# Kernel optimization log

Measured on AMD Instinct MI355X. Metric: run time of the kernel, lower is better.

## Reference

```python
import jax, jax.numpy as jnp
import numpy as np

DIM = 384
PATCH = [(4, 4), (8, 8), (16, 16)]  # (width, height) per channel chunk
B, H, W = 4, 192, 192


def setup_inputs() -> dict:
    key = jax.random.key(0)
    ks = jax.random.split(key, 6)
    c = DIM
    return {
        "rgb": jax.random.normal(ks[0], (B, c, H, W), jnp.float32),
        "fre": jax.random.normal(ks[1], (B, c, H, W), jnp.float32),
        # shared BatchNorm2d (eval-mode affine) applied to both rgb and fre
        "norm_gamma": jnp.ones((c,), jnp.float32),
        "norm_beta": jnp.zeros((c,), jnp.float32),
        "norm_mean": jnp.zeros((c,), jnp.float32),
        "norm_var": jnp.ones((c,), jnp.float32),
        # qv: Conv2d(c, 2c, 1); k: Conv2d(c, c, 1)
        "qv_w": jax.random.normal(ks[2], (2 * c, c), jnp.float32) * 0.02,
        "qv_b": jnp.zeros((2 * c,), jnp.float32),
        "k_w": jax.random.normal(ks[3], (c, c), jnp.float32) * 0.02,
        "k_b": jnp.zeros((c,), jnp.float32),
        # out_conv: Conv2d(c, c, 3, padding=1, bias=False) + BN + LeakyReLU(0.2)
        "oc_w": jax.random.normal(ks[4], (c, c, 3, 3), jnp.float32) * 0.02,
        "oc_gamma": jnp.ones((c,), jnp.float32),
        "oc_beta": jnp.zeros((c,), jnp.float32),
        "oc_mean": jnp.zeros((c,), jnp.float32),
        "oc_var": jnp.ones((c,), jnp.float32),
    }


def _bn(x, g, b, m, v, eps=1e-5):
    scale = g * jax.lax.rsqrt(v + eps)
    return x * scale[None, :, None, None] + (b - m * scale)[None, :, None, None]


def _conv1x1(x, w, b):
    return jnp.einsum('bchw,oc->bohw', x, w) + b[None, :, None, None]


def _win_attn(q, k, v, ww, wh, scale):
    # q,k,v: [b, d, h, w]; window of size (wh x ww)
    b, d, h, w = q.shape
    gh, gw = h // wh, w // ww

    def to_win(t):  # -> [b, gh*gw, wh*ww, d]
        t = t.reshape(b, d, gh, wh, gw, ww).transpose(0, 2, 4, 3, 5, 1)
        return t.reshape(b, gh * gw, wh * ww, d)

    qw, kw, vw = to_win(q), to_win(k), to_win(v)
    attn = jax.nn.softmax((qw * scale) @ kw.swapaxes(-2, -1), axis=-1)
    o = (attn @ vw).reshape(b, gh, gw, wh, ww, d)
    return o.transpose(0, 5, 1, 3, 2, 4).reshape(b, d, h, w)


def reference(rgb, fre, norm_gamma, norm_beta, norm_mean, norm_var,
              qv_w, qv_b, k_w, k_b, oc_w, oc_gamma, oc_beta, oc_mean, oc_var):
    b, c, h, w = rgb.shape
    n = len(PATCH)
    d_k = c // n
    scale = d_k ** (-0.5)

    qv = _conv1x1(_bn(rgb, norm_gamma, norm_beta, norm_mean, norm_var), qv_w, qv_b)
    q, v = qv[:, :c], qv[:, c:]  # reshape(b,2,c,h,w) ordering -> first c = q, next c = v
    k = _conv1x1(_bn(fre, norm_gamma, norm_beta, norm_mean, norm_var), k_w, k_b)

    outs = []
    for i, (ww, wh) in enumerate(PATCH):
        sl = slice(i * d_k, (i + 1) * d_k)
        o = _win_attn(q[:, sl], k[:, sl], v[:, sl], ww, wh, scale) + rgb[:, sl]
        outs.append(o)
    x = jnp.concatenate(outs, axis=1)

    x = jax.lax.conv_general_dilated(x, oc_w, (1, 1), 'SAME',
                                     dimension_numbers=('NCHW', 'OIHW', 'NCHW'))
    x = _bn(x, oc_gamma, oc_beta, oc_mean, oc_var)
    return jnp.where(x >= 0, x, 0.2 * x)  # LeakyReLU(0.2)
```

## Files before the change

### kernel.cpp

```cpp
#include <hip/hip_runtime.h>
#include <stdint.h>

typedef __attribute__((ext_vector_type(8))) short short8;
typedef __attribute__((ext_vector_type(8))) unsigned short ushort8;
typedef __attribute__((ext_vector_type(4))) float f32x4;

#define MFMA(a,b,c) __builtin_amdgcn_mfma_f32_16x16x32_bf16((a),(b),(c),0,0,0)

__device__ __forceinline__ unsigned short f2bf(float f) {
  union { float f; unsigned u; } v; v.f = f;
  unsigned r = v.u + 0x7fffu + ((v.u >> 16) & 1u);
  return (unsigned short)(r >> 16);
}

__device__ __forceinline__ void g2l16(const unsigned short* g, unsigned short* l) {
  __builtin_amdgcn_global_load_lds(
      (const __attribute__((address_space(1))) unsigned int*)(g),
      (__attribute__((address_space(3))) unsigned int*)(l), 16, 0, 0);
}

__device__ __forceinline__ int vswz(int c, int key) {
  return key ^ ((((c >> 3) ^ c) & 7) << 3);
}

__global__ void fold_qvk_kernel(const float* __restrict__ qv_w, const float* __restrict__ qv_b,
                                const float* __restrict__ k_w, const float* __restrict__ k_b,
                                const float* __restrict__ g, const float* __restrict__ be,
                                const float* __restrict__ mu, const float* __restrict__ var,
                                unsigned short* __restrict__ Wq, float* __restrict__ bq,
                                unsigned short* __restrict__ Wk, float* __restrict__ bk) {
  int o = blockIdx.x;
  int t = threadIdx.x;
  bool isq = o < 768;
  int oo = isq ? o : o - 768;
  const float* wrow = isq ? qv_w + (size_t)oo * 384 : k_w + (size_t)oo * 384;
  float mul = (isq && oo < 384) ? 0.08838834764831845f : 1.0f;
  float acc = 0.f;
  for (int c = t; c < 384; c += 128) {
    float sc = g[c] * rsqrtf(var[c] + 1e-5f);
    float sh = be[c] - mu[c] * sc;
    float w = wrow[c];
    acc += w * sh;
    unsigned short wb = f2bf(w * sc * mul);
    if (isq) Wq[(size_t)oo * 384 + c] = wb; else Wk[(size_t)oo * 384 + c] = wb;
  }
#pragma unroll
  for (int m = 1; m < 64; m <<= 1) acc += __shfl_xor(acc, m);
  __shared__ float part[2];
  if ((t & 63) == 0) part[t >> 6] = acc;
  __syncthreads();
  if (t == 0) {
    float b0 = isq ? qv_b[oo] : k_b[oo];
    float bias = (b0 + part[0] + part[1]) * mul;
    if (isq) bq[oo] = bias; else bk[oo] = bias;
  }
}

__global__ void fold_oc_kernel(const float* __restrict__ oc_w,
                               const float* __restrict__ g, const float* __restrict__ be,
                               const float* __restrict__ mu, const float* __restrict__ var,
                               unsigned short* __restrict__ Wc, float* __restrict__ s_oc,
                               float* __restrict__ t_oc) {
  int idx = blockIdx.x * 256 + threadIdx.x;
  if (idx < 384) {
    float sc = g[idx] * rsqrtf(var[idx] + 1e-5f);
    s_oc[idx] = sc;
    t_oc[idx] = be[idx] - mu[idx] * sc;
  }
  if (idx < 384 * 3456) {
    int o = idx / 3456, r = idx % 3456;
    int kq = r / 384, c = r % 384;
    Wc[idx] = f2bf(oc_w[((size_t)o * 384 + c) * 9 + kq]);
  }
}

__launch_bounds__(256)
__global__ void gemm1_kernel(const float* __restrict__ X, const unsigned short* __restrict__ W,
                             const float* __restrict__ bias, unsigned short* __restrict__ Out,
                             int OW, int OT) {
  int bi = blockIdx.x;
  int ot = bi % OT;
  int pt = (bi / OT) % 288;
  int bb = bi / (OT * 288);
  int obase = ot * 128, pbase = pt * 128;
  __shared__ unsigned short As[128 * 40];
  __shared__ unsigned short Bs[128 * 40];
  int tid = threadIdx.x;
  int wv = tid >> 6, lane = tid & 63;
  int l15 = lane & 15, lg = lane >> 4;
  int pw = (wv >> 1) * 64, ow = (wv & 1) * 64;
  f32x4 acc[4][4];
#pragma unroll
  for (int i = 0; i < 4; ++i)
#pragma unroll
    for (int j = 0; j < 4; ++j) acc[i][j] = 0.f;
  const float* Xb = X + (size_t)bb * 384 * 36864;
  int arow = tid >> 1, ahalf = tid & 1;
  int bp = tid & 127, bcg0 = tid >> 7;
  for (int ks = 0; ks < 12; ++ks) {
    int c0 = ks * 32;
    __syncthreads();
    {
      const uint4* s4 = (const uint4*)(W + (size_t)(obase + arow) * 384 + c0 + ahalf * 16);
      uint4 a0 = s4[0], a1 = s4[1];
      uint4* d = (uint4*)&As[arow * 40 + ahalf * 16];
      d[0] = a0; d[1] = a1;
    }
    {
#pragma unroll
      for (int q = 0; q < 2; ++q) {
        int cg = bcg0 + q * 2;
        int cc = c0 + cg * 8;
        const float* src = Xb + (size_t)cc * 36864 + pbase + bp;
        ushort8 t8;
#pragma unroll
        for (int j = 0; j < 8; ++j) t8[j] = f2bf(src[(size_t)j * 36864]);
        *(ushort8*)&Bs[bp * 40 + cg * 8] = t8;
      }
    }
    __syncthreads();
    short8 af[4], bf[4];
#pragma unroll
    for (int f = 0; f < 4; ++f) af[f] = *(const short8*)&Bs[(pw + f * 16 + l15) * 40 + lg * 8];
#pragma unroll
    for (int f = 0; f < 4; ++f) bf[f] = *(const short8*)&As[(ow + f * 16 + l15) * 40 + lg * 8];
#pragma unroll
    for (int fm = 0; fm < 4; ++fm)
#pragma unroll
      for (int fn = 0; fn < 4; ++fn)
        acc[fm][fn] = MFMA(af[fm], bf[fn], acc[fm][fn]);
  }
  unsigned short* Ob = Out + (size_t)bb * 36864 * OW;
#pragma unroll
  for (int fn = 0; fn < 4; ++fn) {
    int o = obase + ow + fn * 16 + l15;
    float bsv = bias[o];
#pragma unroll
    for (int fm = 0; fm < 4; ++fm) {
#pragma unroll
      for (int r = 0; r < 4; ++r) {
        int p = pbase + pw + fm * 16 + lg * 4 + r;
        Ob[(size_t)p * OW + o] = f2bf(acc[fm][fn][r] + bsv);
      }
    }
  }
}

template <int MODE>
__launch_bounds__(256)
__global__ void attn_kernel(const unsigned short* qv, const unsigned short* kx,
                            const float* __restrict__ rgb, unsigned short* xout, int padded) {
  constexpr int GB = MODE * 128;
  constexpr int NKV = (MODE == 2) ? 4 : 1;
  constexpr int NKF = (MODE == 0) ? 1 : 4;
  int bi = blockIdx.x;
  int bb = bi / 576;
  int r5 = bi % 576;
  int tid = threadIdx.x;
  int wv = tid >> 6, lane = tid & 63;
  int l15 = lane & 15, lg = lane >> 4;

  int h0, w0, qtb;
  if (MODE == 0) { int wy = r5 / 12; int wxb = (r5 % 12) * 4; h0 = wy * 4; w0 = wxb * 4; qtb = 0; }
  else if (MODE == 1) { int wy = r5 / 24; int wx = r5 % 24; h0 = wy * 8; w0 = wx * 8; qtb = 0; }
  else { int win = r5 >> 2; int qt = r5 & 3; int wy = win / 12; int wx = win % 12; h0 = wy * 16; w0 = wx * 16; qtb = qt * 64; }

  auto tok2p = [&](int t) -> int {
    if (MODE == 0) { int lw = t >> 4, tt = t & 15; return (h0 + (tt >> 2)) * 192 + w0 + lw * 4 + (tt & 3); }
    else if (MODE == 1) { return (h0 + (t >> 3)) * 192 + w0 + (t & 7); }
    else { return (h0 + (t >> 4)) * 192 + w0 + (t & 15); }
  };

  __shared__ unsigned short Qs[64 * 128];
  __shared__ unsigned short Ks[64 * 128];
  __shared__ unsigned short Vst[128 * 64];
  __shared__ unsigned short Ps[4 * 16 * 72];

  const unsigned short* qvB = qv + (size_t)bb * 36864 * 768;
  const unsigned short* kB = kx + (size_t)bb * 36864 * 384;

  for (int ch = tid; ch < 1024; ch += 256) {
    int tok = ch >> 4, c8 = (ch & 15) << 3;
    int p = tok2p(qtb + tok);
    uint4 v = *(const uint4*)(qvB + (size_t)p * 768 + GB + c8);
    *(uint4*)&Qs[tok * 128 + (c8 ^ ((tok & 7) << 3))] = v;
  }
  __syncthreads();
  short8 qf[4];
  {
    int qrow = wv * 16 + l15;
#pragma unroll
    for (int cs = 0; cs < 4; ++cs)
      qf[cs] = *(const short8*)&Qs[qrow * 128 + ((cs * 32 + lg * 8) ^ ((qrow & 7) << 3))];
  }

  float m[4], s[4];
#pragma unroll
  for (int r = 0; r < 4; ++r) { m[r] = -1e30f; s[r] = 0.f; }
  f32x4 oacc[8];
#pragma unroll
  for (int i = 0; i < 8; ++i) oacc[i] = 0.f;

  for (int kt = 0; kt < NKV; ++kt) {
    __syncthreads();
    for (int ch = tid; ch < 1024; ch += 256) {
      int tok = ch >> 4, c8 = (ch & 15) << 3;
      int p = tok2p(kt * 64 + tok);
      uint4 v = *(const uint4*)(kB + (size_t)p * 384 + GB + c8);
      *(uint4*)&Ks[tok * 128 + (c8 ^ ((tok & 7) << 3))] = v;
    }
    for (int ch = tid; ch < 1024; ch += 256) {
      int key = ch >> 4, c8 = (ch & 15) << 3;
      int p = tok2p(kt * 64 + key);
      ushort8 v = *(const ushort8*)(qvB + (size_t)p * 768 + 384 + GB + c8);
#pragma unroll
      for (int j = 0; j < 8; ++j)
        Vst[(c8 + j) * 64 + vswz(c8 + j, key)] = v[j];
    }
    __syncthreads();

    f32x4 sc[NKF];
#pragma unroll
    for (int kfi = 0; kfi < NKF; ++kfi) {
      int kf = (MODE == 0) ? wv : kfi;
      int krow = kf * 16 + l15;
      f32x4 a; a = 0.f;
#pragma unroll
      for (int cs = 0; cs < 4; ++cs) {
        short8 kfr = *(const short8*)&Ks[krow * 128 + ((cs * 32 + lg * 8) ^ ((krow & 7) << 3))];
        a = MFMA(qf[cs], kfr, a);
      }
      sc[kfi] = a;
    }

    unsigned short* Pw = Ps + wv * (16 * 72);
    float pr[4][NKF];
#pragma unroll
    for (int r = 0; r < 4; ++r) {
      float mx = -1e30f;
#pragma unroll
      for (int kfi = 0; kfi < NKF; ++kfi) mx = fmaxf(mx, sc[kfi][r]);
#pragma unroll
      for (int d = 1; d < 16; d <<= 1) mx = fmaxf(mx, __shfl_xor(mx, d));
      float mn = fmaxf(m[r], mx);
      float f = __expf(m[r] - mn);
      float ls = 0.f;
#pragma unroll
      for (int kfi = 0; kfi < NKF; ++kfi) { float e = __expf(sc[kfi][r] - mn); pr[r][kfi] = e; ls += e; }
#pragma unroll
      for (int d = 1; d < 16; d <<= 1) ls += __shfl_xor(ls, d);
      s[r] = s[r] * f + ls;
      m[r] = mn;
#pragma unroll
      for (int ct = 0; ct < 8; ++ct) oacc[ct][r] *= f;
    }
#pragma unroll
    for (int r = 0; r < 4; ++r) {
      int prow = lg * 4 + r;
#pragma unroll
      for (int kfi = 0; kfi < NKF; ++kfi) {
        int pcol = (MODE == 0) ? l15 : kfi * 16 + l15;
        Pw[prow * 72 + pcol] = f2bf(pr[r][kfi]);
      }
      if (MODE == 0) Pw[prow * 72 + 16 + l15] = 0;
    }
    constexpr int nks = (MODE == 0) ? 1 : 2;
#pragma unroll
    for (int ks = 0; ks < nks; ++ks) {
      short8 pf = *(const short8*)&Pw[l15 * 72 + ks * 32 + lg * 8];
#pragma unroll
      for (int ct = 0; ct < 8; ++ct) {
        int c = ct * 16 + l15;
        short8 vf;
        if (MODE == 0) {
          if (lg < 2) vf = *(const short8*)&Vst[c * 64 + vswz(c, wv * 16 + lg * 8)];
          else vf = 0;
        } else {
          vf = *(const short8*)&Vst[c * 64 + vswz(c, ks * 32 + lg * 8)];
        }
        oacc[ct] = MFMA(pf, vf, oacc[ct]);
      }
    }
  }

  const float* rgbB = rgb + (size_t)bb * 384 * 36864;
  unsigned short* xB = padded ? xout + (size_t)bb * 37636 * 384
                              : xout + (size_t)bb * 36864 * 768;
#pragma unroll
  for (int r = 0; r < 4; ++r) {
    int q64 = wv * 16 + lg * 4 + r;
    int p = tok2p(qtb + q64);
    float inv = 1.0f / s[r];
    size_t rowoff;
    if (padded) {
      int h = p / 192, w = p % 192;
      rowoff = (size_t)((h + 1) * 194 + (w + 1)) * 384;
    } else {
      rowoff = (size_t)p * 768;
    }
#pragma unroll
    for (int ct = 0; ct < 8; ++ct) {
      int c = GB + ct * 16 + l15;
      float val = oacc[ct][r] * inv + rgbB[(size_t)c * 36864 + p];
      xB[rowoff + c] = f2bf(val);
    }
  }
}

__global__ void zero_border_kernel(unsigned short* __restrict__ xpad) {
  int bi = blockIdx.x;
  int bb = bi / 772, i = bi % 772;
  int h, w;
  if (i < 194) { h = 0; w = i; }
  else if (i < 388) { h = 193; w = i - 194; }
  else if (i < 580) { w = 0; h = i - 388 + 1; }
  else { w = 193; h = i - 580 + 1; }
  int t = threadIdx.x;
  if (t < 48) {
    uint4 z = {0, 0, 0, 0};
    uint4* row = (uint4*)(xpad + ((size_t)bb * 37636 + h * 194 + w) * 384);
    row[t] = z;
  }
}

__launch_bounds__(512)
__global__ void conv3d_kernel(const unsigned short* __restrict__ Xp,
                              const unsigned short* __restrict__ Wc,
                              const float* __restrict__ s_oc, const float* __restrict__ t_oc,
                              float* __restrict__ Out) {
  int bid = blockIdx.x;
  int bi = (bid & 7) * 216 + (bid >> 3);
  int pt = bi % 144;
  int ot = (bi / 144) % 3;
  int bb = bi / 432;
  int obase = ot * 128, pbase = pt * 256;
  __shared__ unsigned short Ws2[2][128 * 32];
  __shared__ unsigned short Xs2[2][256 * 32];
  int tid = threadIdx.x;
  int wv = tid >> 6, lane = tid & 63;
  int l15 = lane & 15, lg = lane >> 4;
  int wc = wv & 1, wr = wv >> 1;
  f32x4 acc[4][4];
#pragma unroll
  for (int i = 0; i < 4; ++i)
#pragma unroll
    for (int j = 0; j < 4; ++j) acc[i][j] = 0.f;
  int rl = lane >> 2;
  int csw = (((lane & 3) ^ ((lane >> 3) & 3)) << 3);
  const unsigned short* Ap = Wc + (size_t)(obase + 16 * wv + rl) * 3456 + csw;
  int p0 = pbase + 32 * wv + rl;
  int p1 = p0 + 16;
  const unsigned short* Xb = Xp + (size_t)bb * 37636 * 384;
  const unsigned short* Bp0 = Xb + (size_t)((p0 / 192 + 1) * 194 + (p0 % 192 + 1) - 195) * 384 + csw;
  const unsigned short* Bp1 = Xb + (size_t)((p1 / 192 + 1) * 194 + (p1 % 192 + 1) - 195) * 384 + csw;
  int colsw = ((lg ^ ((l15 >> 1) & 3)) << 3);
  unsigned short* WsW = &Ws2[0][(16 * wv) * 32];
  unsigned short* XsW0 = &Xs2[0][(32 * wv) * 32];
  unsigned short* XsW1 = &Xs2[0][(32 * wv + 16) * 32];
  const int WBUF = 128 * 32, XBUF = 256 * 32;
  g2l16(Ap, WsW);
  g2l16(Bp0, XsW0);
  g2l16(Bp1, XsW1);
  Ap += 32; Bp0 += 32; Bp1 += 32;
  for (int t = 0; t < 108; ++t) {
    int cur = t & 1, nxt = cur ^ 1;
    if (t < 107) {
      g2l16(Ap, WsW + nxt * WBUF);
      g2l16(Bp0, XsW0 + nxt * XBUF);
      g2l16(Bp1, XsW1 + nxt * XBUF);
      Ap += 32; Bp0 += 32; Bp1 += 32;
      if (t == 34 || t == 70) { Bp0 += 73344; Bp1 += 73344; }
      asm volatile("s_waitcnt vmcnt(3)" ::: "memory");
    } else {
      asm volatile("s_waitcnt vmcnt(0)" ::: "memory");
    }
    __builtin_amdgcn_s_barrier();
    __builtin_amdgcn_sched_barrier(0);
    const unsigned short* Wt = &Ws2[cur][0];
    const unsigned short* Xt = &Xs2[cur][0];
    short8 af[4], bf2[4];
#pragma unroll
    for (int f = 0; f < 4; ++f) af[f] = *(const short8*)&Wt[(wc * 64 + f * 16 + l15) * 32 + colsw];
#pragma unroll
    for (int f = 0; f < 4; ++f) bf2[f] = *(const short8*)&Xt[(wr * 64 + f * 16 + l15) * 32 + colsw];
#pragma unroll
    for (int fm = 0; fm < 4; ++fm)
#pragma unroll
      for (int fn = 0; fn < 4; ++fn)
        acc[fm][fn] = MFMA(af[fm], bf2[fn], acc[fm][fn]);
    __builtin_amdgcn_s_barrier();
    __builtin_amdgcn_sched_barrier(0);
  }
  float* Ob = Out + (size_t)bb * 384 * 36864;
#pragma unroll
  for (int fm = 0; fm < 4; ++fm) {
#pragma unroll
    for (int r = 0; r < 4; ++r) {
      int o = obase + wc * 64 + fm * 16 + lg * 4 + r;
      float sv = s_oc[o], tv = t_oc[o];
#pragma unroll
      for (int fn = 0; fn < 4; ++fn) {
        int p = pbase + wr * 64 + fn * 16 + l15;
        float y = acc[fm][fn][r] * sv + tv;
        Ob[(size_t)o * 36864 + p] = (y >= 0.f) ? y : 0.2f * y;
      }
    }
  }
}

__launch_bounds__(256)
__global__ void conv3_kernel(const unsigned short* __restrict__ X,
                             const unsigned short* __restrict__ Wc,
                             const float* __restrict__ s_oc, const float* __restrict__ t_oc,
                             float* __restrict__ Out) {
  int bi = blockIdx.x;
  int pt = bi % 288;
  int ot = (bi / 288) % 3;
  int bb = bi / 864;
  int obase = ot * 128, pbase = pt * 128;
  __shared__ unsigned short As[128 * 40];
  __shared__ unsigned short Bs[128 * 40];
  int tid = threadIdx.x;
  int wv = tid >> 6, lane = tid & 63;
  int l15 = lane & 15, lg = lane >> 4;
  int ow = (wv & 1) * 64, pw = (wv >> 1) * 64;
  f32x4 acc[4][4];
#pragma unroll
  for (int i = 0; i < 4; ++i)
#pragma unroll
    for (int j = 0; j < 4; ++j) acc[i][j] = 0.f;
  int arow = tid >> 1, ahalf = tid & 1;
  int sp = pbase + arow;
  int sh = sp / 192, sw = sp % 192;
  const unsigned short* Xb = X + (size_t)bb * 36864 * 768;
  for (int ksi = 0; ksi < 108; ++ksi) {
    int kq = ksi / 12;
    int c0 = (ksi % 12) * 32;
    int dh = kq / 3 - 1, dw = kq % 3 - 1;
    __syncthreads();
    {
      const uint4* s4 = (const uint4*)(Wc + (size_t)(obase + arow) * 3456 + kq * 384 + c0 + ahalf * 16);
      uint4 a0 = s4[0], a1 = s4[1];
      uint4* d = (uint4*)&As[arow * 40 + ahalf * 16];
      d[0] = a0; d[1] = a1;
    }
    {
      int hh = sh + dh, ww2 = sw + dw;
      uint4 b0 = {0, 0, 0, 0}, b1 = {0, 0, 0, 0};
      if ((unsigned)hh < 192u && (unsigned)ww2 < 192u) {
        const uint4* s4 = (const uint4*)(Xb + (size_t)(hh * 192 + ww2) * 768 + c0 + ahalf * 16);
        b0 = s4[0]; b1 = s4[1];
      }
      uint4* d = (uint4*)&Bs[arow * 40 + ahalf * 16];
      d[0] = b0; d[1] = b1;
    }
    __syncthreads();
    short8 af[4], bf2[4];
#pragma unroll
    for (int f = 0; f < 4; ++f) af[f] = *(const short8*)&As[(ow + f * 16 + l15) * 40 + lg * 8];
#pragma unroll
    for (int f = 0; f < 4; ++f) bf2[f] = *(const short8*)&Bs[(pw + f * 16 + l15) * 40 + lg * 8];
#pragma unroll
    for (int fm = 0; fm < 4; ++fm)
#pragma unroll
      for (int fn = 0; fn < 4; ++fn)
        acc[fm][fn] = MFMA(af[fm], bf2[fn], acc[fm][fn]);
  }
  float* Ob = Out + (size_t)bb * 384 * 36864;
#pragma unroll
  for (int fm = 0; fm < 4; ++fm) {
#pragma unroll
    for (int r = 0; r < 4; ++r) {
      int o = obase + ow + fm * 16 + lg * 4 + r;
      float sv = s_oc[o], tv = t_oc[o];
#pragma unroll
      for (int fn = 0; fn < 4; ++fn) {
        int p = pbase + pw + fn * 16 + l15;
        float y = acc[fm][fn][r] * sv + tv;
        Ob[(size_t)o * 36864 + p] = (y >= 0.f) ? y : 0.2f * y;
      }
    }
  }
}

extern "C" void kernel_launch(void* const* d_in, const int* in_sizes, int n_in,
                              void* d_out, int out_size, void* d_ws, size_t ws_size,
                              hipStream_t stream) {
  const float* rgb  = (const float*)d_in[0];
  const float* fre  = (const float*)d_in[1];
  const float* ng   = (const float*)d_in[2];
  const float* nb   = (const float*)d_in[3];
  const float* nm   = (const float*)d_in[4];
  const float* nv   = (const float*)d_in[5];
  const float* qv_w = (const float*)d_in[6];
  const float* qv_b = (const float*)d_in[7];
  const float* k_w  = (const float*)d_in[8];
  const float* k_b  = (const float*)d_in[9];
  const float* oc_w = (const float*)d_in[10];
  const float* oc_g = (const float*)d_in[11];
  const float* oc_b = (const float*)d_in[12];
  const float* oc_m = (const float*)d_in[13];
  const float* oc_v = (const float*)d_in[14];

  char* ws = (char*)d_ws;
  const size_t QV_B   = 226492416;
  const size_t K_B    = 113246208;
  const size_t XPAD_B = 115617792;
  size_t off = 0;
  unsigned short* qvbuf = (unsigned short*)(ws + off); off += QV_B;
  unsigned short* kbuf  = (unsigned short*)(ws + off); off += K_B;
  size_t xpad_off = off;
  bool fast = (ws_size >= xpad_off + XPAD_B + 4 * 1024 * 1024);
  unsigned short* xpad = (unsigned short*)(ws + xpad_off);
  if (fast) off += XPAD_B;
  unsigned short* Wq = (unsigned short*)(ws + off); off += 589824;
  unsigned short* Wk = (unsigned short*)(ws + off); off += 294912;
  unsigned short* Wc = (unsigned short*)(ws + off); off += 2654208;
  float* bq  = (float*)(ws + off); off += 3072;
  float* bk  = (float*)(ws + off); off += 1536;
  float* soc = (float*)(ws + off); off += 1536;
  float* toc = (float*)(ws + off); off += 1536;
  float* out = (float*)d_out;

  if (fast) zero_border_kernel<<<dim3(4 * 772), dim3(64), 0, stream>>>(xpad);
  fold_qvk_kernel<<<dim3(1152), dim3(128), 0, stream>>>(qv_w, qv_b, k_w, k_b, ng, nb, nm, nv, Wq, bq, Wk, bk);
  fold_oc_kernel<<<dim3(5184), dim3(256), 0, stream>>>(oc_w, oc_g, oc_b, oc_m, oc_v, Wc, soc, toc);
  gemm1_kernel<<<dim3(4 * 288 * 6), dim3(256), 0, stream>>>(rgb, Wq, bq, qvbuf, 768, 6);
  gemm1_kernel<<<dim3(4 * 288 * 3), dim3(256), 0, stream>>>(fre, Wk, bk, kbuf, 384, 3);
  unsigned short* xdst = fast ? xpad : qvbuf;
  int padded = fast ? 1 : 0;
  attn_kernel<0><<<dim3(2304), dim3(256), 0, stream>>>(qvbuf, kbuf, rgb, xdst, padded);
  attn_kernel<1><<<dim3(2304), dim3(256), 0, stream>>>(qvbuf, kbuf, rgb, xdst, padded);
  attn_kernel<2><<<dim3(2304), dim3(256), 0, stream>>>(qvbuf, kbuf, rgb, xdst, padded);
  if (fast)
    conv3d_kernel<<<dim3(1728), dim3(512), 0, stream>>>(xpad, Wc, soc, toc, out);
  else
    conv3_kernel<<<dim3(4 * 3 * 288), dim3(256), 0, stream>>>(qvbuf, Wc, soc, toc, out);
}
```

Before: 1.324 ms.

## Pre-transpose inputs to NHWC bf16 and use a pipelined GEMM for 1x1 convs

Adds a transpose kernel that converts rgb and fre from NCHW fp32 to NHWC bf16, then runs the 1x1 convolutions with a new double-buffered, LDS-DMA GEMM modelled on the 3x3 conv kernel. The attention residual now reads the bf16 NHWC copy of rgb instead of strided fp32 reads. The block order of the 3x3 conv is also changed so that neighbouring blocks share pixel tiles. In exchange it adds two extra transpose passes, needs more workspace, and rounds the residual to bf16.

```diff
diff --git a/kernel.cpp b/kernel.cpp
--- a/kernel.cpp
+++ b/kernel.cpp
@@ -12,6 +12,10 @@
   unsigned r = v.u + 0x7fffu + ((v.u >> 16) & 1u);
   return (unsigned short)(r >> 16);
 }
+__device__ __forceinline__ float bf2f(unsigned short s) {
+  union { unsigned u; float f; } v; v.u = ((unsigned)s) << 16;
+  return v.f;
+}
 
 __device__ __forceinline__ void g2l16(const unsigned short* g, unsigned short* l) {
   __builtin_amdgcn_global_load_lds(
@@ -21,6 +25,29 @@
 
 __device__ __forceinline__ int vswz(int c, int key) {
   return key ^ ((((c >> 3) ^ c) & 7) << 3);
+}
+
+__global__ void nhwc_kernel(const float* __restrict__ src, unsigned short* __restrict__ dst) {
+  __shared__ unsigned short T[64][72];
+  int p0 = blockIdx.x * 64, c0 = blockIdx.y * 64, bb = blockIdx.z;
+  const float* S = src + (size_t)bb * 384 * 36864;
+  unsigned short* D = dst + (size_t)bb * 36864 * 384;
+  int t = threadIdx.x;
+  int pl = (t & 15) * 4;
+  int r0 = t >> 4;
+#pragma unroll
+  for (int k = 0; k < 4; ++k) {
+    int c = r0 + 16 * k;
+    float4 v = *(const float4*)&S[(size_t)(c0 + c) * 36864 + p0 + pl];
+    T[pl + 0][c] = f2bf(v.x); T[pl + 1][c] = f2bf(v.y);
+    T[pl + 2][c] = f2bf(v.z); T[pl + 3][c] = f2bf(v.w);
+  }
+  __syncthreads();
+  int row = t >> 2, ch = (t & 3) * 16;
+  ushort8 a = *(const ushort8*)&T[row][ch];
+  ushort8 b = *(const ushort8*)&T[row][ch + 8];
+  uint4* d = (uint4*)&D[(size_t)(p0 + row) * 384 + c0 + ch];
+  d[0] = *(uint4*)&a; d[1] = *(uint4*)&b;
 }
 
 __global__ void fold_qvk_kernel(const float* __restrict__ qv_w, const float* __restrict__ qv_b,
@@ -74,6 +101,85 @@
   }
 }
 
+__launch_bounds__(512)
+__global__ void gemm1n_kernel(const unsigned short* __restrict__ XN, const unsigned short* __restrict__ W,
+                              const float* __restrict__ bias, unsigned short* __restrict__ Out,
+                              int OW, int OT) {
+  int nwg = gridDim.x;
+  int bid = blockIdx.x;
+  int bi = (bid & 7) * (nwg >> 3) + (bid >> 3);
+  int ot = bi % OT;
+  int pt = (bi / OT) % 144;
+  int bb = bi / (OT * 144);
+  int obase = ot * 128, pbase = pt * 256;
+  __shared__ unsigned short Ws2[2][128 * 32];
+  __shared__ unsigned short Xs2[2][256 * 32];
+  int tid = threadIdx.x;
+  int wv = tid >> 6, lane = tid & 63;
+  int l15 = lane & 15, lg = lane >> 4;
+  int wc = wv & 1, wr = wv >> 1;
+  f32x4 acc[4][4];
+#pragma unroll
+  for (int i = 0; i < 4; ++i)
+#pragma unroll
+    for (int j = 0; j < 4; ++j) acc[i][j] = 0.f;
+  int rl = lane >> 2;
+  int csw = (((lane & 3) ^ ((lane >> 3) & 3)) << 3);
+  const unsigned short* Ap = W + (size_t)(obase + 16 * wv + rl) * 384 + csw;
+  const unsigned short* XbN = XN + (size_t)bb * 36864 * 384;
+  const unsigned short* Bp0 = XbN + (size_t)(pbase + 32 * wv + rl) * 384 + csw;
+  const unsigned short* Bp1 = Bp0 + (size_t)16 * 384;
+  int colsw = ((lg ^ ((l15 >> 1) & 3)) << 3);
+  unsigned short* WsW = &Ws2[0][(16 * wv) * 32];
+  unsigned short* XsW0 = &Xs2[0][(32 * wv) * 32];
+  unsigned short* XsW1 = &Xs2[0][(32 * wv + 16) * 32];
+  const int WBUF = 128 * 32, XBUF = 256 * 32;
+  g2l16(Ap, WsW); g2l16(Bp0, XsW0); g2l16(Bp1, XsW1);
+  Ap += 32; Bp0 += 32; Bp1 += 32;
+  for (int t = 0; t < 12; ++t) {
+    int cur = t & 1, nxt = cur ^ 1;
+    if (t < 11) {
+      g2l16(Ap, WsW + nxt * WBUF);
+      g2l16(Bp0, XsW0 + nxt * XBUF);
+      g2l16(Bp1, XsW1 + nxt * XBUF);
+      Ap += 32; Bp0 += 32; Bp1 += 32;
+      asm volatile("s_waitcnt vmcnt(3)" ::: "memory");
+    } else {
+      asm volatile("s_waitcnt vmcnt(0)" ::: "memory");
+    }
+    __builtin_amdgcn_s_barrier();
+    __builtin_amdgcn_sched_barrier(0);
+    const unsigned short* Wt = &Ws2[cur][0];
+    const unsigned short* Xt = &Xs2[cur][0];
+    short8 af[4], bf[4];
+#pragma unroll
+    for (int f = 0; f < 4; ++f) af[f] = *(const short8*)&Xt[(wr * 64 + f * 16 + l15) * 32 + colsw];
+#pragma unroll
+    for (int f = 0; f < 4; ++f) bf[f] = *(const short8*)&Wt[(wc * 64 + f * 16 + l15) * 32 + colsw];
+#pragma unroll
+    for (int fm = 0; fm < 4; ++fm)
+#pragma unroll
+      for (int fn = 0; fn < 4; ++fn)
+        acc[fm][fn] = MFMA(af[fm], bf[fn], acc[fm][fn]);
+    __builtin_amdgcn_s_barrier();
+    __builtin_amdgcn_sched_barrier(0);
+  }
+  unsigned short* Ob = Out + (size_t)bb * 36864 * OW;
+#pragma unroll
+  for (int fn = 0; fn < 4; ++fn) {
+    int o = obase + wc * 64 + fn * 16 + l15;
+    float bsv = bias[o];
+#pragma unroll
+    for (int fm = 0; fm < 4; ++fm) {
+#pragma unroll
+      for (int r = 0; r < 4; ++r) {
+        int p = pbase + wr * 64 + fm * 16 + lg * 4 + r;
+        Ob[(size_t)p * OW + o] = f2bf(acc[fm][fn][r] + bsv);
+      }
+    }
+  }
+}
+
 __launch_bounds__(256)
 __global__ void gemm1_kernel(const float* __restrict__ X, const unsigned short* __restrict__ W,
                              const float* __restrict__ bias, unsigned short* __restrict__ Out,
@@ -149,7 +255,8 @@
 template <int MODE>
 __launch_bounds__(256)
 __global__ void attn_kernel(const unsigned short* qv, const unsigned short* kx,
-                            const float* __restrict__ rgb, unsigned short* xout, int padded) {
+                            const float* __restrict__ rgb, const unsigned short* __restrict__ rgbn,
+                            unsigned short* xout, int padded) {
   constexpr int GB = MODE * 128;
   constexpr int NKV = (MODE == 2) ? 4 : 1;
   constexpr int NKF = (MODE == 0) ? 1 : 4;
@@ -284,6 +391,7 @@
   }
 
   const float* rgbB = rgb + (size_t)bb * 384 * 36864;
+  const unsigned short* rgbNB = rgbn + (size_t)bb * 36864 * 384;
   unsigned short* xB = padded ? xout + (size_t)bb * 37636 * 384
                               : xout + (size_t)bb * 36864 * 768;
 #pragma unroll
@@ -301,7 +409,8 @@
 #pragma unroll
     for (int ct = 0; ct < 8; ++ct) {
       int c = GB + ct * 16 + l15;
-      float val = oacc[ct][r] * inv + rgbB[(size_t)c * 36864 + p];
+      float res = padded ? bf2f(rgbNB[(size_t)p * 384 + c]) : rgbB[(size_t)c * 36864 + p];
+      float val = oacc[ct][r] * inv + res;
       xB[rowoff + c] = f2bf(val);
     }
   }
@@ -330,8 +439,8 @@
                               float* __restrict__ Out) {
   int bid = blockIdx.x;
   int bi = (bid & 7) * 216 + (bid >> 3);
-  int pt = bi % 144;
-  int ot = (bi / 144) % 3;
+  int ot = bi % 3;
+  int pt = (bi / 3) % 144;
   int bb = bi / 432;
   int obase = ot * 128, pbase = pt * 256;
   __shared__ unsigned short Ws2[2][128 * 32];
@@ -358,9 +467,7 @@
   unsigned short* XsW0 = &Xs2[0][(32 * wv) * 32];
   unsigned short* XsW1 = &Xs2[0][(32 * wv + 16) * 32];
   const int WBUF = 128 * 32, XBUF = 256 * 32;
-  g2l16(Ap, WsW);
-  g2l16(Bp0, XsW0);
-  g2l16(Bp1, XsW1);
+  g2l16(Ap, WsW); g2l16(Bp0, XsW0); g2l16(Bp1, XsW1);
   Ap += 32; Bp0 += 32; Bp1 += 32;
   for (int t = 0; t < 108; ++t) {
     int cur = t & 1, nxt = cur ^ 1;
@@ -506,13 +613,16 @@
   const size_t QV_B   = 226492416;
   const size_t K_B    = 113246208;
   const size_t XPAD_B = 115617792;
+  const size_t RGBN_B = 113246208;
   size_t off = 0;
   unsigned short* qvbuf = (unsigned short*)(ws + off); off += QV_B;
   unsigned short* kbuf  = (unsigned short*)(ws + off); off += K_B;
-  size_t xpad_off = off;
-  bool fast = (ws_size >= xpad_off + XPAD_B + 4 * 1024 * 1024);
-  unsigned short* xpad = (unsigned short*)(ws + xpad_off);
-  if (fast) off += XPAD_B;
+  size_t dyn_off = off;
+  unsigned short* xpad = (unsigned short*)(ws + dyn_off);
+  unsigned short* rgbN = (unsigned short*)(ws + dyn_off + XPAD_B);
+  const size_t WEIGHTS_B = 589824 + 294912 + 2654208 + 3072 + 1536 + 1536 + 1536;
+  bool fast = (ws_size >= dyn_off + XPAD_B + RGBN_B + WEIGHTS_B);
+  if (fast) off += XPAD_B + RGBN_B;
   unsigned short* Wq = (unsigned short*)(ws + off); off += 589824;
   unsigned short* Wk = (unsigned short*)(ws + off); off += 294912;
   unsigned short* Wc = (unsigned short*)(ws + off); off += 2654208;
@@ -522,18 +632,26 @@
   float* toc = (float*)(ws + off); off += 1536;
   float* out = (float*)d_out;
 
-  if (fast) zero_border_kernel<<<dim3(4 * 772), dim3(64), 0, stream>>>(xpad);
   fold_qvk_kernel<<<dim3(1152), dim3(128), 0, stream>>>(qv_w, qv_b, k_w, k_b, ng, nb, nm, nv, Wq, bq, Wk, bk);
   fold_oc_kernel<<<dim3(5184), dim3(256), 0, stream>>>(oc_w, oc_g, oc_b, oc_m, oc_v, Wc, soc, toc);
-  gemm1_kernel<<<dim3(4 * 288 * 6), dim3(256), 0, stream>>>(rgb, Wq, bq, qvbuf, 768, 6);
-  gemm1_kernel<<<dim3(4 * 288 * 3), dim3(256), 0, stream>>>(fre, Wk, bk, kbuf, 384, 3);
-  unsigned short* xdst = fast ? xpad : qvbuf;
-  int padded = fast ? 1 : 0;
-  attn_kernel<0><<<dim3(2304), dim3(256), 0, stream>>>(qvbuf, kbuf, rgb, xdst, padded);
-  attn_kernel<1><<<dim3(2304), dim3(256), 0, stream>>>(qvbuf, kbuf, rgb, xdst, padded);
-  attn_kernel<2><<<dim3(2304), dim3(256), 0, stream>>>(qvbuf, kbuf, rgb, xdst, padded);
-  if (fast)
+
+  if (fast) {
+    unsigned short* freN = xpad;
+    nhwc_kernel<<<dim3(576, 6, 4), dim3(256), 0, stream>>>(rgb, rgbN);
+    nhwc_kernel<<<dim3(576, 6, 4), dim3(256), 0, stream>>>(fre, freN);
+    gemm1n_kernel<<<dim3(3456), dim3(512), 0, stream>>>(rgbN, Wq, bq, qvbuf, 768, 6);
+    gemm1n_kernel<<<dim3(1728), dim3(512), 0, stream>>>(freN, Wk, bk, kbuf, 384, 3);
+    zero_border_kernel<<<dim3(4 * 772), dim3(64), 0, stream>>>(xpad);
+    attn_kernel<0><<<dim3(2304), dim3(256), 0, stream>>>(qvbuf, kbuf, rgb, rgbN, xpad, 1);
+    attn_kernel<1><<<dim3(2304), dim3(256), 0, stream>>>(qvbuf, kbuf, rgb, rgbN, xpad, 1);
+    attn_kernel<2><<<dim3(2304), dim3(256), 0, stream>>>(qvbuf, kbuf, rgb, rgbN, xpad, 1);
     conv3d_kernel<<<dim3(1728), dim3(512), 0, stream>>>(xpad, Wc, soc, toc, out);
-  else
+  } else {
+    gemm1_kernel<<<dim3(4 * 288 * 6), dim3(256), 0, stream>>>(rgb, Wq, bq, qvbuf, 768, 6);
+    gemm1_kernel<<<dim3(4 * 288 * 3), dim3(256), 0, stream>>>(fre, Wk, bk, kbuf, 384, 3);
+    attn_kernel<0><<<dim3(2304), dim3(256), 0, stream>>>(qvbuf, kbuf, rgb, qvbuf, qvbuf, 0);
+    attn_kernel<1><<<dim3(2304), dim3(256), 0, stream>>>(qvbuf, kbuf, rgb, qvbuf, qvbuf, 0);
+    attn_kernel<2><<<dim3(2304), dim3(256), 0, stream>>>(qvbuf, kbuf, rgb, qvbuf, qvbuf, 0);
     conv3_kernel<<<dim3(4 * 3 * 288), dim3(256), 0, stream>>>(qvbuf, Wc, soc, toc, out);
-}
+  }
+}
```

New measurement: 1.219 ms. 8.0% less time.
